# Kernel tuning notes

Hardware: AMD Instinct MI355X
Metric: run time of the kernel (lower is better)

Reference implementation:

```python
import jax, jax.numpy as jnp
import numpy as np

N_HEADS = 16
NEG = -1000000000.0  # masked_fill value from the original code


def setup_inputs() -> dict:
    key = jax.random.key(0)
    ks = jax.random.split(key, 7)
    D = 1024
    x = jax.random.normal(ks[0], (2, 2048, D), dtype=jnp.float32)
    s = 1.0 / np.sqrt(D)
    Wq = jax.random.normal(ks[1], (D, D), dtype=jnp.float32) * s
    bq = jax.random.normal(ks[2], (D,), dtype=jnp.float32) * 0.01
    Wk = jax.random.normal(ks[3], (D, D), dtype=jnp.float32) * s
    bk = jax.random.normal(ks[4], (D,), dtype=jnp.float32) * 0.01
    Wv = jax.random.normal(ks[5], (D, D), dtype=jnp.float32) * s
    bv = jax.random.normal(ks[6], (D,), dtype=jnp.float32) * 0.01
    return {"x": x, "Wq": Wq, "bq": bq, "Wk": Wk, "bk": bk, "Wv": Wv, "bv": bv}


def reference(x, Wq, bq, Wk, bk, Wv, bv):
    B, S, D = x.shape
    H = N_HEADS
    dh = D // H
    # nn.Linear: x @ W.T + b
    Q = (x @ Wq.T + bq).reshape(B, S, H, dh)
    K = (x @ Wk.T + bk).reshape(B, S, H, dh)
    V = (x @ Wv.T + bv).reshape(B, S, H, dh)
    # NOTE: original scales by sqrt(n_heads), not sqrt(d_head) -- faithful.
    scale = jnp.asarray(H, x.dtype) ** 0.5
    scores = jnp.einsum('bqhd,bkhd->bhqk', Q, K) / scale  # [B,H,S,S]
    # Original: mask = triu(ones, diag=1); scores.masked_fill(mask == 0, -1e9)
    # i.e. positions where the STRICT-UPPER mask is False (lower triangle incl.
    # diagonal) get -1e9. Faithful reproduction of that (buggy) behavior.
    triu = jnp.triu(jnp.ones((S, S), dtype=bool), k=1)  # [S,S]
    scores = jnp.where(triu[None, None, :, :], scores, jnp.asarray(NEG, x.dtype))
    probs = jax.nn.softmax(scores, axis=-1)
    # dropout is identity at inference
    out = jnp.einsum('bhqk,bkhd->bqhd', probs, V).reshape(B, S, D)
    return out
```

## Files before the change

### kernel.cpp

```cpp
#include <hip/hip_runtime.h>
#include <stdint.h>

typedef unsigned short u16;
typedef __attribute__((ext_vector_type(8))) short bf16x8;
typedef __attribute__((ext_vector_type(4))) float floatx4;

#define MFMA16(a, b, c) __builtin_amdgcn_mfma_f32_16x16x32_bf16(a, b, c, 0, 0, 0)
#define MEMFENCE asm volatile("" ::: "memory")
#define WAIT_VM0 asm volatile("s_waitcnt vmcnt(0)" ::: "memory")
#define WAIT_LGKM0 asm volatile("s_waitcnt lgkmcnt(0)" ::: "memory")

#if __has_builtin(__builtin_amdgcn_exp2f)
#define EXP2(x) __builtin_amdgcn_exp2f(x)
#else
#define EXP2(x) __expf(0.6931471805599453f * (x))
#endif

__device__ __forceinline__ u16 f2bf(float f) {
  unsigned u = __builtin_bit_cast(unsigned, f);
  return (u16)((u + 0x7FFFu + ((u >> 16) & 1u)) >> 16);
}
__device__ __forceinline__ u16 f2bf_hu(float f) {
  return (u16)((__builtin_bit_cast(unsigned, f) + 0x8000u) >> 16);
}
__device__ __forceinline__ float bf2f(u16 v) {
  return __builtin_bit_cast(float, (unsigned)v << 16);
}

__device__ __forceinline__ void glds16(void* lds, const void* g) {
  __builtin_amdgcn_global_load_lds((const __attribute__((address_space(1))) void*)g,
                                   (__attribute__((address_space(3))) void*)lds,
                                   16, 0, 0);
}

__global__ __launch_bounds__(256) void cvt_all(
    const float* __restrict__ x, const float* __restrict__ w0,
    const float* __restrict__ w1, const float* __restrict__ w2,
    u16* __restrict__ xb, u16* __restrict__ Wb) {
  const int bid = blockIdx.x;
  const float* src;
  u16* dst;
  int i;
  if (bid < 4096) {
    src = x; dst = xb; i = bid * 256 + threadIdx.x;
  } else {
    const int z = (bid - 4096) >> 10;
    src = (z == 0) ? w0 : (z == 1) ? w1 : w2;
    dst = Wb + (size_t)z * (1024 * 1024);
    i = ((bid - 4096) & 1023) * 256 + threadIdx.x;
  }
  float4 f = reinterpret_cast<const float4*>(src)[i];
  ushort4 o;
  o.x = f2bf(f.x); o.y = f2bf(f.y); o.z = f2bf(f.z); o.w = f2bf(f.w);
  reinterpret_cast<ushort4*>(dst)[i] = o;
}

__global__ __launch_bounds__(256, 3) void qkv_gemm(
    const u16* __restrict__ xb, const u16* __restrict__ Wb,
    const float* __restrict__ bq, const float* __restrict__ bk,
    const float* __restrict__ bv,
    u16* __restrict__ Qb, u16* __restrict__ Kb, u16* __restrict__ VTb) {
  __shared__ __attribute__((aligned(16))) u16 smem[2 * 128 * 64];
  u16* As = smem;
  u16* Bs = smem + 128 * 64;

  const int tid = threadIdx.x;
  const int w = tid >> 6, lane = tid & 63;
  const int lo = lane & 15, quad = lane >> 4;
  const int which = blockIdx.z;
  const int m0 = blockIdx.x * 128, n0 = blockIdx.y * 128;

  const u16* W = Wb + (size_t)which * (1024 * 1024);
  const int wm = (w >> 1) * 64, wn = (w & 1) * 64;

  floatx4 acc[4][4];
  for (int i = 0; i < 4; ++i)
    for (int j = 0; j < 4; ++j) acc[i][j] = (floatx4)0.f;

  const int arow = lane >> 3;
  const int aswz = ((lane & 7) ^ arow) * 8;

  for (int kt = 0; kt < 16; ++kt) {
    const int k0 = kt * 64;
    for (int j = 0; j < 4; ++j) {
      const int seg = w * 4 + j;
      glds16(As + seg * 512, xb + (size_t)(m0 + seg * 8 + arow) * 1024 + k0 + aswz);
      glds16(Bs + seg * 512, W + (size_t)(n0 + seg * 8 + arow) * 1024 + k0 + aswz);
    }
    __syncthreads();
    for (int kk = 0; kk < 2; ++kk) {
      const int swz = ((kk * 4 + quad) ^ (lo & 7)) * 8;
      bf16x8 af[4], bfr[4];
      for (int it = 0; it < 4; ++it)
        af[it] = *reinterpret_cast<const bf16x8*>(As + (wm + it * 16 + lo) * 64 + swz);
      for (int jt = 0; jt < 4; ++jt)
        bfr[jt] = *reinterpret_cast<const bf16x8*>(Bs + (wn + jt * 16 + lo) * 64 + swz);
      for (int it = 0; it < 4; ++it)
        for (int jt = 0; jt < 4; ++jt)
          acc[it][jt] = MFMA16(af[it], bfr[jt], acc[it][jt]);
    }
    __syncthreads();
  }

  const float* bias = (which == 0) ? bq : (which == 1) ? bk : bv;
  float bb[4];
  for (int jt = 0; jt < 4; ++jt) bb[jt] = bias[n0 + wn + jt * 16 + lo];
  const int b = m0 >> 11;

  if (which < 2) {
    const float scl = (which == 0) ? 0.36067376022224085f : 1.0f;
    u16* Tw = smem + w * (16 * 72);
    const int hblk = (n0 + wn) >> 6;
    u16* dst = ((which == 0) ? Qb : Kb) +
               ((size_t)(b * 16 + hblk) * 2048 + ((m0 & 2047) + wm)) * 64;
    for (int it = 0; it < 4; ++it) {
      for (int jt = 0; jt < 4; ++jt)
        for (int r = 0; r < 4; ++r) {
          const int m = quad * 4 + r, col = jt * 16 + lo;
          Tw[m * 72 + (((col >> 3) ^ (m & 7)) * 8) + (col & 7)] =
              f2bf((acc[it][jt][r] + bb[jt]) * scl);
        }
      MEMFENCE;
      for (int rd = 0; rd < 2; ++rd) {
        const int sr = rd * 8 + (lane >> 3), d8 = lane & 7;
        bf16x8 v = *reinterpret_cast<const bf16x8*>(Tw + sr * 72 + ((d8 ^ (sr & 7)) * 8));
        *reinterpret_cast<bf16x8*>(dst + (size_t)(it * 16 + sr) * 64 + d8 * 8) = v;
      }
      MEMFENCE;
    }
  } else {
    for (int pass = 0; pass < 2; ++pass) {
      if ((wm >> 6) == pass) {
        for (int it = 0; it < 4; ++it)
          for (int jt = 0; jt < 4; ++jt)
            for (int r = 0; r < 4; ++r) {
              const int n = wn + jt * 16 + lo;
              const int m = it * 16 + quad * 4 + r;
              smem[n * 72 + (((m >> 3) ^ (n & 7)) * 8) + (m & 7)] =
                  f2bf(acc[it][jt][r] + bb[jt]);
            }
      }
      __syncthreads();
      for (int rd = 0; rd < 4; ++rd) {
        const int n = (tid >> 3) + rd * 32, m8 = tid & 7;
        bf16x8 v = *reinterpret_cast<const bf16x8*>(smem + n * 72 + ((m8 ^ (n & 7)) * 8));
        const int ng = n0 + n, h = ng >> 6, d = ng & 63;
        const int s = (m0 & 2047) + pass * 64 + m8 * 8;
        *reinterpret_cast<bf16x8*>(VTb + ((size_t)(b * 16 + h) * 64 + d) * 2048 + s) = v;
      }
      __syncthreads();
    }
  }
}

__global__ __launch_bounds__(64, 2) void attn(
    const u16* __restrict__ Qb, const u16* __restrict__ Kb,
    const u16* __restrict__ VTb, float* __restrict__ out) {
  __shared__ __attribute__((aligned(16))) u16 Ks[64 * 64];
  __shared__ __attribute__((aligned(16))) u16 Vs[64 * 64];
  __shared__ __attribute__((aligned(16))) u16 Pt[2][16 * 64];

  const int L = blockIdx.x;
  const int bh = L & 31;
  const int qtA = L >> 5;

  const int lane = threadIdx.x & 63;
  const int lo = lane & 15, quad = lane >> 4;

  const u16* Qh = Qb + (size_t)bh * (2048 * 64);
  const u16* Kh = Kb + (size_t)bh * (2048 * 64);
  const u16* Vh = VTb + (size_t)bh * (64 * 2048);

  const int srow8 = lane >> 3, sblk = lane & 7;
  const int sswz = (sblk ^ srow8) * 8;
  const int b = bh >> 4, hh = bh & 15;

#define STAGE(kt)                                                             \
  for (int j = 0; j < 8; ++j) {                                               \
    glds16(&Ks[j * 512], Kh + (size_t)((kt) * 64 + j * 8 + srow8) * 64 + sswz); \
    glds16(&Vs[j * 512], Vh + (size_t)(j * 8 + srow8) * 2048 + (kt) * 64 + sswz); \
  }

  { STAGE(qtA >> 1); }

  for (int p = 0; p < 2; ++p) {
    const int qtp = (p == 0) ? qtA : 63 - qtA;
    const int kstart = qtp >> 1;
    const int n = 32 - kstart;

    int qrow[2];
    bf16x8 qf[2][2];
    for (int s = 0; s < 2; ++s) {
      qrow[s] = qtp * 32 + s * 16 + lo;
      qf[s][0] = *reinterpret_cast<const bf16x8*>(Qh + (size_t)qrow[s] * 64 + quad * 8);
      qf[s][1] = *reinterpret_cast<const bf16x8*>(Qh + (size_t)qrow[s] * 64 + 32 + quad * 8);
    }

    float lrun[2] = {0.f, 0.f};
    floatx4 acc[2][4];
    for (int s = 0; s < 2; ++s)
      for (int dt = 0; dt < 4; ++dt) acc[s][dt] = (floatx4)0.f;

    for (int i = 0; i < n; ++i) {
      const int kt = kstart + i;
      WAIT_VM0;
      MEMFENCE;

      floatx4 sc[2][4];
      for (int s = 0; s < 2; ++s)
        for (int t = 0; t < 4; ++t) sc[s][t] = (floatx4)0.f;
      bf16x8 va[2][4];
      for (int kk = 0; kk < 2; ++kk) {
        const int swz = ((kk * 4 + quad) ^ (lo & 7)) * 8;
        for (int t = 0; t < 4; ++t) {
          bf16x8 ka = *reinterpret_cast<const bf16x8*>(Ks + (t * 16 + lo) * 64 + swz);
          sc[0][t] = MFMA16(ka, qf[0][kk], sc[0][t]);
          sc[1][t] = MFMA16(ka, qf[1][kk], sc[1][t]);
        }
        for (int dt = 0; dt < 4; ++dt)
          va[kk][dt] = *reinterpret_cast<const bf16x8*>(Vs + (dt * 16 + lo) * 64 + swz);
      }

      const bool maskp = (i == 0);
      for (int s = 0; s < 2; ++s) {
        u16* ptw = &Pt[s][0];
        for (int t = 0; t < 4; ++t) {
          float p0 = EXP2(sc[s][t][0]), p1 = EXP2(sc[s][t][1]);
          float p2 = EXP2(sc[s][t][2]), p3 = EXP2(sc[s][t][3]);
          if (maskp) {
            const int key = kt * 64 + t * 16 + quad * 4;
            p0 = (key + 0 > qrow[s]) ? p0 : 0.f;
            p1 = (key + 1 > qrow[s]) ? p1 : 0.f;
            p2 = (key + 2 > qrow[s]) ? p2 : 0.f;
            p3 = (key + 3 > qrow[s]) ? p3 : 0.f;
          }
          lrun[s] += (p0 + p1) + (p2 + p3);
          ushort4 pk;
          pk.x = f2bf_hu(p0); pk.y = f2bf_hu(p1);
          pk.z = f2bf_hu(p2); pk.w = f2bf_hu(p3);
          u16* pdst = ptw + lo * 64 +
                      (((2 * t + (quad >> 1)) ^ (lo & 7)) * 8) + (quad & 1) * 4;
          *reinterpret_cast<ushort4*>(pdst) = pk;
        }
      }
      MEMFENCE;

      bf16x8 pb[2][2];
      for (int kk = 0; kk < 2; ++kk) {
        const int pswz = ((kk * 4 + quad) ^ (lo & 7)) * 8;
        pb[0][kk] = *reinterpret_cast<const bf16x8*>(&Pt[0][lo * 64] + pswz);
        pb[1][kk] = *reinterpret_cast<const bf16x8*>(&Pt[1][lo * 64] + pswz);
      }
      WAIT_LGKM0;
      MEMFENCE;

      if (i + 1 < n) { STAGE(kt + 1); }
      else if (p == 0) { STAGE((63 - qtA) >> 1); }

      for (int kk = 0; kk < 2; ++kk)
        for (int dt = 0; dt < 4; ++dt) {
          acc[0][dt] = MFMA16(va[kk][dt], pb[0][kk], acc[0][dt]);
          acc[1][dt] = MFMA16(va[kk][dt], pb[1][kk], acc[1][dt]);
        }
    }

    for (int s = 0; s < 2; ++s) {
      float l = lrun[s];
      l += __shfl_xor(l, 16);
      l += __shfl_xor(l, 32);
      if (l != 0.f) {
        const float rl = 1.f / l;
        float* op = out + ((size_t)(b * 2048 + qrow[s])) * 1024 + hh * 64 + quad * 4;
        for (int dt = 0; dt < 4; ++dt) {
          float4 o4;
          o4.x = acc[s][dt][0] * rl; o4.y = acc[s][dt][1] * rl;
          o4.z = acc[s][dt][2] * rl; o4.w = acc[s][dt][3] * rl;
          *reinterpret_cast<float4*>(op + dt * 16) = o4;
        }
      }
    }
  }
#undef STAGE
}

__global__ __launch_bounds__(256) void fix2047(const u16* __restrict__ VTb,
                                               float* __restrict__ out) {
  const int bh = blockIdx.x;
  const u16* Vh = VTb + (size_t)bh * (64 * 2048);
  const int t = threadIdx.x;
  const int d = t >> 2, j = t & 3;
  float s = 0.f;
  const u16* row = Vh + (size_t)d * 2048 + j * 512;
  for (int i = 0; i < 64; ++i) {
    bf16x8 v = *reinterpret_cast<const bf16x8*>(row + i * 8);
    for (int e = 0; e < 8; ++e) s += bf2f((u16)v[e]);
  }
  s += __shfl_xor(s, 1);
  s += __shfl_xor(s, 2);
  if (j == 0) {
    const int b = bh >> 4, h = bh & 15;
    out[((size_t)(b * 2048 + 2047)) * 1024 + h * 64 + d] = s * (1.f / 2048.f);
  }
}

extern "C" void kernel_launch(void* const* d_in, const int* in_sizes, int n_in,
                              void* d_out, int out_size, void* d_ws, size_t ws_size,
                              hipStream_t stream) {
  const float* x  = (const float*)d_in[0];
  const float* Wq = (const float*)d_in[1];
  const float* bq = (const float*)d_in[2];
  const float* Wk = (const float*)d_in[3];
  const float* bk = (const float*)d_in[4];
  const float* Wv = (const float*)d_in[5];
  const float* bv = (const float*)d_in[6];
  float* out = (float*)d_out;

  char* ws = (char*)d_ws;
  u16* xb  = (u16*)(ws);
  u16* Wb  = (u16*)(ws + (8u << 20));
  u16* Qb  = (u16*)(ws + (14u << 20));
  u16* Kb  = (u16*)(ws + (22u << 20));
  u16* VTb = (u16*)(ws + (30u << 20));

  cvt_all<<<7168, 256, 0, stream>>>(x, Wq, Wk, Wv, xb, Wb);
  qkv_gemm<<<dim3(32, 8, 3), 256, 0, stream>>>(xb, Wb, bq, bk, bv, Qb, Kb, VTb);
  attn<<<dim3(1024), 64, 0, stream>>>(Qb, Kb, VTb, out);
  fix2047<<<dim3(32), 256, 0, stream>>>(VTb, out);
}
```

Measured before the change: 171.0 us.

## Load K/V tiles directly into registers with double-buffering, drop LDS staging

The attention kernel stops staging K and V tiles through shared memory with global-to-LDS copies. Each lane now loads its MFMA operand fragments straight from global memory into two register buffers, prefetching the next tile while the current one is computed. The paired-query-tile load balancing (one block handling tile q and tile 63-q) is also removed in favour of one query tile per block, doubling the grid to 2048 blocks. This removes the LDS round trip and the full vmcnt wait, but raises register pressure, relies on the L2/cache for K/V reuse, and leaves block workloads uneven.

Measured after the change: 194.0 us. +13.5%, slower.

```diff
diff --git a/kernel.cpp b/kernel.cpp
--- a/kernel.cpp
+++ b/kernel.cpp
@@ -7,7 +7,6 @@
 
 #define MFMA16(a, b, c) __builtin_amdgcn_mfma_f32_16x16x32_bf16(a, b, c, 0, 0, 0)
 #define MEMFENCE asm volatile("" ::: "memory")
-#define WAIT_VM0 asm volatile("s_waitcnt vmcnt(0)" ::: "memory")
 #define WAIT_LGKM0 asm volatile("s_waitcnt lgkmcnt(0)" ::: "memory")
 
 #if __has_builtin(__builtin_amdgcn_exp2f)
@@ -156,13 +155,13 @@
 __global__ __launch_bounds__(64, 2) void attn(
     const u16* __restrict__ Qb, const u16* __restrict__ Kb,
     const u16* __restrict__ VTb, float* __restrict__ out) {
-  __shared__ __attribute__((aligned(16))) u16 Ks[64 * 64];
-  __shared__ __attribute__((aligned(16))) u16 Vs[64 * 64];
   __shared__ __attribute__((aligned(16))) u16 Pt[2][16 * 64];
 
   const int L = blockIdx.x;
   const int bh = L & 31;
-  const int qtA = L >> 5;
+  const int qt = L >> 5;
+  const int kstart = qt >> 1;
+  const int n = 32 - kstart;
 
   const int lane = threadIdx.x & 63;
   const int lo = lane & 15, quad = lane >> 4;
@@ -171,116 +170,113 @@
   const u16* Kh = Kb + (size_t)bh * (2048 * 64);
   const u16* Vh = VTb + (size_t)bh * (64 * 2048);
 
-  const int srow8 = lane >> 3, sblk = lane & 7;
-  const int sswz = (sblk ^ srow8) * 8;
+  int qrow[2];
+  bf16x8 qf[2][2];
+  for (int s = 0; s < 2; ++s) {
+    qrow[s] = qt * 32 + s * 16 + lo;
+    qf[s][0] = *reinterpret_cast<const bf16x8*>(Qh + (size_t)qrow[s] * 64 + quad * 8);
+    qf[s][1] = *reinterpret_cast<const bf16x8*>(Qh + (size_t)qrow[s] * 64 + 32 + quad * 8);
+  }
+
+  float lrun[2] = {0.f, 0.f};
+  floatx4 acc[2][4];
+  for (int s = 0; s < 2; ++s)
+    for (int dt = 0; dt < 4; ++dt) acc[s][dt] = (floatx4)0.f;
+
+#define LOADK(D, kt_)                                                         \
+  _Pragma("unroll") for (int t = 0; t < 4; ++t) {                             \
+    const u16* kp = Kh + (size_t)((kt_) * 64 + t * 16 + lo) * 64 + quad * 8;  \
+    D[t] = *reinterpret_cast<const bf16x8*>(kp);                              \
+    D[4 + t] = *reinterpret_cast<const bf16x8*>(kp + 32);                     \
+  }
+#define LOADV(D, kt_)                                                         \
+  _Pragma("unroll") for (int c = 0; c < 8; ++c) {                             \
+    D[c] = *reinterpret_cast<const bf16x8*>(                                  \
+        Vh + (size_t)((c & 3) * 16 + lo) * 2048 + (kt_) * 64 +                \
+        (c >> 2) * 32 + quad * 8);                                            \
+  }
+
+#define ITER(KC, VC, KN, VN)                                                  \
+  {                                                                           \
+    const int kt = kstart + i;                                                \
+    floatx4 sc[2][4];                                                         \
+    _Pragma("unroll") for (int s = 0; s < 2; ++s)                             \
+      _Pragma("unroll") for (int t = 0; t < 4; ++t) sc[s][t] = (floatx4)0.f;  \
+    _Pragma("unroll") for (int kk = 0; kk < 2; ++kk)                          \
+      _Pragma("unroll") for (int t = 0; t < 4; ++t) {                         \
+        sc[0][t] = MFMA16(KC[kk * 4 + t], qf[0][kk], sc[0][t]);               \
+        sc[1][t] = MFMA16(KC[kk * 4 + t], qf[1][kk], sc[1][t]);               \
+      }                                                                       \
+    if (i + 1 < n) { LOADK(KN, kt + 1); LOADV(VN, kt + 1); }                  \
+    const bool maskp = (i == 0);                                              \
+    _Pragma("unroll") for (int s = 0; s < 2; ++s) {                           \
+      u16* ptw = &Pt[s][0];                                                   \
+      _Pragma("unroll") for (int t = 0; t < 4; ++t) {                         \
+        float p0 = EXP2(sc[s][t][0]), p1 = EXP2(sc[s][t][1]);                 \
+        float p2 = EXP2(sc[s][t][2]), p3 = EXP2(sc[s][t][3]);                 \
+        if (maskp) {                   \
+          const int key = kt * 64 + t * 16 + quad * 4;                        \
+          p0 = (key + 0 > qrow[s]) ? p0 : 0.f;                                \
+          p1 = (key + 1 > qrow[s]) ? p1 : 0.f;                                \
+          p2 = (key + 2 > qrow[s]) ? p2 : 0.f;                                \
+          p3 = (key + 3 > qrow[s]) ? p3 : 0.f;                                \
+        }                                                                     \
+        lrun[s] += (p0 + p1) + (p2 + p3);                                     \
+        ushort4 pk;                                                           \
+        pk.x = f2bf_hu(p0); pk.y = f2bf_hu(p1);                               \
+        pk.z = f2bf_hu(p2); pk.w = f2bf_hu(p3);                               \
+        u16* pdst = ptw + lo * 64 +                                           \
+                    (((2 * t + (quad >> 1)) ^ (lo & 7)) * 8) + (quad & 1) * 4;\
+        *reinterpret_cast<ushort4*>(pdst) = pk;                               \
+      }                                                                       \
+    }                                                                         \
+    MEMFENCE;              \
+    bf16x8 pb[2][2];                                                          \
+    _Pragma("unroll") for (int kk = 0; kk < 2; ++kk) {                        \
+      const int pswz = ((kk * 4 + quad) ^ (lo & 7)) * 8;                      \
+      pb[0][kk] = *reinterpret_cast<const bf16x8*>(&Pt[0][lo * 64] + pswz);   \
+      pb[1][kk] = *reinterpret_cast<const bf16x8*>(&Pt[1][lo * 64] + pswz);   \
+    }                                                                         \
+    WAIT_LGKM0;               \
+    MEMFENCE;                                                                 \
+    _Pragma("unroll") for (int kk = 0; kk < 2; ++kk)                          \
+      _Pragma("unroll") for (int dt = 0; dt < 4; ++dt) {                      \
+        acc[0][dt] = MFMA16(VC[kk * 4 + dt], pb[0][kk], acc[0][dt]);          \
+        acc[1][dt] = MFMA16(VC[kk * 4 + dt], pb[1][kk], acc[1][dt]);          \
+      }                                                                       \
+    ++i;                                                                      \
+  }
+
+  bf16x8 kA[8], vA[8], kB[8], vB[8];
+  LOADK(kA, kstart);
+  LOADV(vA, kstart);
+  int i = 0;
+  while (true) {
+    ITER(kA, vA, kB, vB);
+    if (i >= n) break;
+    ITER(kB, vB, kA, vA);
+    if (i >= n) break;
+  }
+#undef ITER
+#undef LOADK
+#undef LOADV
+
   const int b = bh >> 4, hh = bh & 15;
-
-#define STAGE(kt)                                                             \
-  for (int j = 0; j < 8; ++j) {                                               \
-    glds16(&Ks[j * 512], Kh + (size_t)((kt) * 64 + j * 8 + srow8) * 64 + sswz); \
-    glds16(&Vs[j * 512], Vh + (size_t)(j * 8 + srow8) * 2048 + (kt) * 64 + sswz); \
-  }
-
-  { STAGE(qtA >> 1); }
-
-  for (int p = 0; p < 2; ++p) {
-    const int qtp = (p == 0) ? qtA : 63 - qtA;
-    const int kstart = qtp >> 1;
-    const int n = 32 - kstart;
-
-    int qrow[2];
-    bf16x8 qf[2][2];
-    for (int s = 0; s < 2; ++s) {
-      qrow[s] = qtp * 32 + s * 16 + lo;
-      qf[s][0] = *reinterpret_cast<const bf16x8*>(Qh + (size_t)qrow[s] * 64 + quad * 8);
-      qf[s][1] = *reinterpret_cast<const bf16x8*>(Qh + (size_t)qrow[s] * 64 + 32 + quad * 8);
-    }
-
-    float lrun[2] = {0.f, 0.f};
-    floatx4 acc[2][4];
-    for (int s = 0; s < 2; ++s)
-      for (int dt = 0; dt < 4; ++dt) acc[s][dt] = (floatx4)0.f;
-
-    for (int i = 0; i < n; ++i) {
-      const int kt = kstart + i;
-      WAIT_VM0;
-      MEMFENCE;
-
-      floatx4 sc[2][4];
-      for (int s = 0; s < 2; ++s)
-        for (int t = 0; t < 4; ++t) sc[s][t] = (floatx4)0.f;
-      bf16x8 va[2][4];
-      for (int kk = 0; kk < 2; ++kk) {
-        const int swz = ((kk * 4 + quad) ^ (lo & 7)) * 8;
-        for (int t = 0; t < 4; ++t) {
-          bf16x8 ka = *reinterpret_cast<const bf16x8*>(Ks + (t * 16 + lo) * 64 + swz);
-          sc[0][t] = MFMA16(ka, qf[0][kk], sc[0][t]);
-          sc[1][t] = MFMA16(ka, qf[1][kk], sc[1][t]);
-        }
-        for (int dt = 0; dt < 4; ++dt)
-          va[kk][dt] = *reinterpret_cast<const bf16x8*>(Vs + (dt * 16 + lo) * 64 + swz);
+  for (int s = 0; s < 2; ++s) {
+    float l = lrun[s];
+    l += __shfl_xor(l, 16);
+    l += __shfl_xor(l, 32);
+    if (l != 0.f) {
+      const float rl = 1.f / l;
+      float* op = out + ((size_t)(b * 2048 + qrow[s])) * 1024 + hh * 64 + quad * 4;
+      for (int dt = 0; dt < 4; ++dt) {
+        float4 o4;
+        o4.x = acc[s][dt][0] * rl; o4.y = acc[s][dt][1] * rl;
+        o4.z = acc[s][dt][2] * rl; o4.w = acc[s][dt][3] * rl;
+        *reinterpret_cast<float4*>(op + dt * 16) = o4;
       }
-
-      const bool maskp = (i == 0);
-      for (int s = 0; s < 2; ++s) {
-        u16* ptw = &Pt[s][0];
-        for (int t = 0; t < 4; ++t) {
-          float p0 = EXP2(sc[s][t][0]), p1 = EXP2(sc[s][t][1]);
-          float p2 = EXP2(sc[s][t][2]), p3 = EXP2(sc[s][t][3]);
-          if (maskp) {
-            const int key = kt * 64 + t * 16 + quad * 4;
-            p0 = (key + 0 > qrow[s]) ? p0 : 0.f;
-            p1 = (key + 1 > qrow[s]) ? p1 : 0.f;
-            p2 = (key + 2 > qrow[s]) ? p2 : 0.f;
-            p3 = (key + 3 > qrow[s]) ? p3 : 0.f;
-          }
-          lrun[s] += (p0 + p1) + (p2 + p3);
-          ushort4 pk;
-          pk.x = f2bf_hu(p0); pk.y = f2bf_hu(p1);
-          pk.z = f2bf_hu(p2); pk.w = f2bf_hu(p3);
-          u16* pdst = ptw + lo * 64 +
-                      (((2 * t + (quad >> 1)) ^ (lo & 7)) * 8) + (quad & 1) * 4;
-          *reinterpret_cast<ushort4*>(pdst) = pk;
-        }
-      }
-      MEMFENCE;
-
-      bf16x8 pb[2][2];
-      for (int kk = 0; kk < 2; ++kk) {
-        const int pswz = ((kk * 4 + quad) ^ (lo & 7)) * 8;
-        pb[0][kk] = *reinterpret_cast<const bf16x8*>(&Pt[0][lo * 64] + pswz);
-        pb[1][kk] = *reinterpret_cast<const bf16x8*>(&Pt[1][lo * 64] + pswz);
-      }
-      WAIT_LGKM0;
-      MEMFENCE;
-
-      if (i + 1 < n) { STAGE(kt + 1); }
-      else if (p == 0) { STAGE((63 - qtA) >> 1); }
-
-      for (int kk = 0; kk < 2; ++kk)
-        for (int dt = 0; dt < 4; ++dt) {
-          acc[0][dt] = MFMA16(va[kk][dt], pb[0][kk], acc[0][dt]);
-          acc[1][dt] = MFMA16(va[kk][dt], pb[1][kk], acc[1][dt]);
-        }
-    }
-
-    for (int s = 0; s < 2; ++s) {
-      float l = lrun[s];
-      l += __shfl_xor(l, 16);
-      l += __shfl_xor(l, 32);
-      if (l != 0.f) {
-        const float rl = 1.f / l;
-        float* op = out + ((size_t)(b * 2048 + qrow[s])) * 1024 + hh * 64 + quad * 4;
-        for (int dt = 0; dt < 4; ++dt) {
-          float4 o4;
-          o4.x = acc[s][dt][0] * rl; o4.y = acc[s][dt][1] * rl;
-          o4.z = acc[s][dt][2] * rl; o4.w = acc[s][dt][3] * rl;
-          *reinterpret_cast<float4*>(op + dt * 16) = o4;
-        }
-      }
-    }
-  }
-#undef STAGE
+    }
+  }
 }
 
 __global__ __launch_bounds__(256) void fix2047(const u16* __restrict__ VTb,
@@ -324,6 +320,6 @@
 
   cvt_all<<<7168, 256, 0, stream>>>(x, Wq, Wk, Wv, xb, Wb);
   qkv_gemm<<<dim3(32, 8, 3), 256, 0, stream>>>(xb, Wb, bq, bk, bv, Qb, Kb, VTb);
-  attn<<<dim3(1024), 64, 0, stream>>>(Qb, Kb, VTb, out);
+  attn<<<dim3(2048), 64, 0, stream>>>(Qb, Kb, VTb, out);
   fix2047<<<dim3(32), 256, 0, stream>>>(VTb, out);
 }
```
